# Performance work log

Hardware: AMD Instinct MI355X
Metric: run time of the kernel (lower is better)

The kernel has to match this reference:

```python
import jax, jax.numpy as jnp
import numpy as np

M_MOL = 8192      # number of molecules
A_ATOMS = 32      # atoms per molecule (uniform ragged groups)
N_FEAT = 128      # schnet n_atom_basis


def setup_inputs() -> dict:
    key = jax.random.key(0)
    sr = jax.random.normal(key, (M_MOL * A_ATOMS, N_FEAT), dtype=jnp.float32)
    # idx_m: sorted molecule index per atom, uniform group sizes
    idx_m = jnp.repeat(jnp.arange(M_MOL, dtype=jnp.int32), A_ATOMS)
    return {"scalar_representation": sr, "idx_m": idx_m}


def reference(scalar_representation, idx_m):
    # maxm = int(idx_m[-1]) + 1 in the torch code; groups are uniform here so
    # torch.split over bincount == a simple reshape into [M, A, F].
    maxm = int(idx_m[-1]) + 1
    n_atoms = scalar_representation.shape[0]
    a = n_atoms // maxm
    sr = scalar_representation.reshape(maxm, a, -1)          # [M, A, F]
    # per-molecule correlation (Gram) matrix: c = sr @ sr.T
    c = jnp.einsum('maf,mbf->mab', sr, sr)                    # [M, A, A]
    # eigvalsh returns ascending eigenvalues; torch code takes [0] (smallest)
    eigvals = jnp.linalg.eigvalsh(c)                          # [M, A]
    return eigvals[:, 0]                                      # [M]
```

## Files before the change

kernel.cpp:

```cpp
#include <hip/hip_runtime.h>
#include <hip/hip_bf16.h>

#define DEVINL __device__ __forceinline__

typedef __attribute__((ext_vector_type(8))) short short8;
typedef __attribute__((ext_vector_type(4))) float f32x4;

DEVINL float rcp_f(float x) { return __builtin_amdgcn_rcpf(x); }

#define LDS_FENCE() __asm__ volatile("" ::: "memory")

template<int CTRL>
DEVINL float dpp_mov(float x) {
  return __int_as_float(__builtin_amdgcn_update_dpp(
      0, __float_as_int(x), CTRL, 0xF, 0xF, true));
}
DEVINL float group_sum(float x) {
  x += dpp_mov<0xB1>(x);
  x += dpp_mov<0x4E>(x);
  x += dpp_mov<0x141>(x);
  x += dpp_mov<0x140>(x);
  return x;
}
DEVINL float group_min(float x) {
  x = fminf(x, dpp_mov<0xB1>(x));
  x = fminf(x, dpp_mov<0x4E>(x));
  x = fminf(x, dpp_mov<0x141>(x));
  x = fminf(x, dpp_mov<0x140>(x));
  return x;
}
DEVINL float group_max(float x) {
  x = fmaxf(x, dpp_mov<0xB1>(x));
  x = fmaxf(x, dpp_mov<0x4E>(x));
  x = fmaxf(x, dpp_mov<0x141>(x));
  x = fmaxf(x, dpp_mov<0x140>(x));
  return x;
}

DEVINL short bf_hi(float f, float& rem) {
  unsigned u = __float_as_uint(f);
  unsigned rh = (u + 0x8000u) >> 16;
  rem = f - __uint_as_float(rh << 16);
  return (short)rh;
}
DEVINL short bf_of(float f) {
  return (short)((__float_as_uint(f) + 0x8000u) >> 16);
}
DEVINL void cvt_hilo(float4 fa, float4 fb, short8& h, short8& lo) {
  float rm;
  h[0] = bf_hi(fa.x, rm); lo[0] = bf_of(rm);
  h[1] = bf_hi(fa.y, rm); lo[1] = bf_of(rm);
  h[2] = bf_hi(fa.z, rm); lo[2] = bf_of(rm);
  h[3] = bf_hi(fa.w, rm); lo[3] = bf_of(rm);
  h[4] = bf_hi(fb.x, rm); lo[4] = bf_of(rm);
  h[5] = bf_hi(fb.y, rm); lo[5] = bf_of(rm);
  h[6] = bf_hi(fb.z, rm); lo[6] = bf_of(rm);
  h[7] = bf_hi(fb.w, rm); lo[7] = bf_of(rm);
}
DEVINL f32x4 mfma_bf16(short8 a, short8 b, f32x4 c) {
  return __builtin_amdgcn_mfma_f32_16x16x32_bf16(a, b, c, 0, 0, 0);
}

template<int K>
DEVINL void house_step(float (&r0)[32], float (&r1)[32], int l, int lane,
                       float* vbuf, float* pbuf, float* dbuf, float* ebuf) {
  constexpr int C0 = (K + 1) / 4;
  constexpr int PE = (K + 1) & 3;

  float xm0, xm1;
  if constexpr (K < 15) xm0 = (l > K) ? r0[K] : 0.0f;
  else                  xm0 = 0.0f;
  if constexpr (K < 16) xm1 = r1[K];
  else                  xm1 = (l > K - 16) ? r1[K] : 0.0f;

  vbuf[l] = xm0; vbuf[l + 16] = xm1;
  LDS_FENCE();

  float xsrc = (K + 1 < 16) ? xm0 : xm1;
  float x0 = __shfl(xsrc, (lane & 48) + ((K + 1) & 15), 64);
  float nn = group_sum(xm0 * xm0 + xm1 * xm1);

  float4 vc[8];
  #pragma unroll
  for (int c = C0; c < 8; ++c) vc[c] = *(const float4*)(vbuf + 4 * c);

  float alpha = -copysignf(sqrtf(nn), x0);
  float denom = nn - alpha * x0;
  float beta = (denom > 1e-20f) ? rcp_f(denom) : 0.0f;

  float v0, v1;
  if constexpr (K + 1 < 16) {
    v0 = xm0 - ((l == K + 1) ? alpha : 0.0f);
    v1 = xm1;
  } else {
    v0 = 0.0f;
    v1 = xm1 - ((l == K + 1 - 16) ? alpha : 0.0f);
  }
  if constexpr (PE == 0)      vc[C0].x -= alpha;
  else if constexpr (PE == 1) vc[C0].y -= alpha;
  else if constexpr (PE == 2) vc[C0].z -= alpha;
  else                        vc[C0].w -= alpha;

  float p0 = 0.0f;
  if constexpr (K < 15) {
    float a0 = 0.0f, a1 = 0.0f;
    #pragma unroll
    for (int c = C0; c < 8; ++c) {
      a0 = fmaf(r0[4 * c + 0], vc[c].x, a0); a1 = fmaf(r0[4 * c + 1], vc[c].y, a1);
      a0 = fmaf(r0[4 * c + 2], vc[c].z, a0); a1 = fmaf(r0[4 * c + 3], vc[c].w, a1);
    }
    p0 = a0 + a1;
  }
  float b0 = 0.0f, b1 = 0.0f;
  #pragma unroll
  for (int c = C0; c < 8; ++c) {
    b0 = fmaf(r1[4 * c + 0], vc[c].x, b0); b1 = fmaf(r1[4 * c + 1], vc[c].y, b1);
    b0 = fmaf(r1[4 * c + 2], vc[c].z, b0); b1 = fmaf(r1[4 * c + 3], vc[c].w, b1);
  }
  float p1 = b0 + b1;

  pbuf[l] = p0; pbuf[l + 16] = p1;
  LDS_FENCE();
  float G = group_sum(v0 * p0 + v1 * p1);
  float c2 = 0.5f * beta * beta * G;

  float s_p0 = 0.0f, s_v0 = 0.0f;
  if constexpr (K < 15) {
    bool act0 = (l > K);
    s_p0 = beta * v0;
    s_v0 = act0 ? fmaf(-2.0f * c2, v0, beta * p0) : 0.0f;
  }
  float s_p1 = beta * v1;
  float s_v1;
  if constexpr (K < 16) s_v1 = fmaf(-2.0f * c2, v1, beta * p1);
  else                  s_v1 = (l > K - 16) ? fmaf(-2.0f * c2, v1, beta * p1) : 0.0f;

  #pragma unroll
  for (int c = C0; c < 8; ++c) {
    float4 pc = *(const float4*)(pbuf + 4 * c);
    if constexpr (K < 15) {
      r0[4 * c + 0] -= s_p0 * pc.x + s_v0 * vc[c].x;
      r0[4 * c + 1] -= s_p0 * pc.y + s_v0 * vc[c].y;
      r0[4 * c + 2] -= s_p0 * pc.z + s_v0 * vc[c].z;
      r0[4 * c + 3] -= s_p0 * pc.w + s_v0 * vc[c].w;
    }
    r1[4 * c + 0] -= s_p1 * pc.x + s_v1 * vc[c].x;
    r1[4 * c + 1] -= s_p1 * pc.y + s_v1 * vc[c].y;
    r1[4 * c + 2] -= s_p1 * pc.z + s_v1 * vc[c].z;
    r1[4 * c + 3] -= s_p1 * pc.w + s_v1 * vc[c].w;
  }

  if constexpr (K < 16) {
    if (l == K) { dbuf[K] = r0[K]; ebuf[K] = alpha; }
  } else {
    if (l == K - 16) { dbuf[K] = r1[K]; ebuf[K] = alpha; }
  }
}

template<int K>
DEVINL void house_all(float (&r0)[32], float (&r1)[32], int l, int lane,
                      float* vbuf, float* pbuf, float* dbuf, float* ebuf) {
  house_step<K>(r0, r1, l, lane, vbuf, pbuf, dbuf, ebuf);
  if constexpr (K < 30) house_all<K + 1>(r0, r1, l, lane, vbuf, pbuf, dbuf, ebuf);
}

__global__ __launch_bounds__(256) void Correlation_85134841741354_kernel(
    const float* __restrict__ A, float* __restrict__ out, int M) {
  const int lane = threadIdx.x & 63;
  const int wave = threadIdx.x >> 6;
  const int q    = lane >> 4;
  const int t    = lane & 15;
  const int molbase = blockIdx.x * 16 + wave * 4;
  if (molbase >= M) return;

  __shared__ float ldsT[4][4][32 * 36 + 8];

  #pragma unroll 1
  for (int g = 0; g < 4; ++g) {
    const float* Am = A + (size_t)(molbase + g) * (32 * 128);
    f32x4 acc00 = {0.f, 0.f, 0.f, 0.f}, acc01 = {0.f, 0.f, 0.f, 0.f};
    f32x4 acc10 = {0.f, 0.f, 0.f, 0.f}, acc11 = {0.f, 0.f, 0.f, 0.f};
    #pragma unroll
    for (int c = 0; c < 4; ++c) {
      const float* pr0 = Am + t * 128        + 32 * c + 8 * q;
      const float* pr1 = Am + (t + 16) * 128 + 32 * c + 8 * q;
      float4 fa0 = *(const float4*)(pr0);
      float4 fb0 = *(const float4*)(pr0 + 4);
      float4 fa1 = *(const float4*)(pr1);
      float4 fb1 = *(const float4*)(pr1 + 4);
      short8 h0, l0, h1, l1;
      cvt_hilo(fa0, fb0, h0, l0);
      cvt_hilo(fa1, fb1, h1, l1);
      acc00 = mfma_bf16(h0, h0, acc00); acc00 = mfma_bf16(h0, l0, acc00); acc00 = mfma_bf16(l0, h0, acc00);
      acc01 = mfma_bf16(h0, h1, acc01); acc01 = mfma_bf16(h0, l1, acc01); acc01 = mfma_bf16(l0, h1, acc01);
      acc10 = mfma_bf16(h1, h0, acc10); acc10 = mfma_bf16(h1, l0, acc10); acc10 = mfma_bf16(l1, h0, acc10);
      acc11 = mfma_bf16(h1, h1, acc11); acc11 = mfma_bf16(h1, l1, acc11); acc11 = mfma_bf16(l1, h1, acc11);
    }
    float* tg = &ldsT[wave][g][0];
    #pragma unroll
    for (int reg = 0; reg < 4; ++reg) {
      tg[(4 * q + reg) * 36 + t]           = acc00[reg];
      tg[(4 * q + reg) * 36 + 16 + t]      = acc01[reg];
      tg[(16 + 4 * q + reg) * 36 + t]      = acc10[reg];
      tg[(16 + 4 * q + reg) * 36 + 16 + t] = acc11[reg];
    }
  }
  LDS_FENCE();

  float* tq = &ldsT[wave][q][0];
  float r0[32], r1[32];
  #pragma unroll
  for (int c = 0; c < 8; ++c) {
    float4 a = *(const float4*)(tq + t * 36 + 4 * c);
    r0[4 * c + 0] = a.x; r0[4 * c + 1] = a.y;
    r0[4 * c + 2] = a.z; r0[4 * c + 3] = a.w;
    float4 b = *(const float4*)(tq + (t + 16) * 36 + 4 * c);
    r1[4 * c + 0] = b.x; r1[4 * c + 1] = b.y;
    r1[4 * c + 2] = b.z; r1[4 * c + 3] = b.w;
  }
  LDS_FENCE();

  float* vbuf = tq;
  float* pbuf = tq + 40;
  float* dbuf = tq + 80;
  float* ebuf = tq + 120;

  house_all<0>(r0, r1, t, lane, vbuf, pbuf, dbuf, ebuf);
  if (t == 15) { dbuf[31] = r1[31]; ebuf[31] = 0.0f; }
  LDS_FENCE();

  float d0 = dbuf[t], d1 = dbuf[t + 16];
  float eh0 = ebuf[t];
  float el0 = (t > 0) ? ebuf[t - 1] : 0.0f;
  float eh1 = ebuf[t + 16];
  float el1 = ebuf[t + 15];
  float rad0 = fabsf(eh0) + fabsf(el0);
  float rad1 = fabsf(eh1) + fabsf(el1);
  float glo = group_min(fminf(d0 - rad0, d1 - rad1));
  float ghi = group_max(fmaxf(d0 + rad0, d1 + rad1));
  float lo = fmaxf(glo - 1e-3f, 0.0f);
  float hi = ghi + 1e-3f;

  float vd[32], ve2[32];
  #pragma unroll
  for (int c = 0; c < 8; ++c) {
    float4 dc = *(const float4*)(dbuf + 4 * c);
    float4 ec = *(const float4*)(ebuf + 4 * c);
    vd[4 * c + 0] = dc.x; vd[4 * c + 1] = dc.y;
    vd[4 * c + 2] = dc.z; vd[4 * c + 3] = dc.w;
    ve2[4 * c + 0] = ec.x * ec.x; ve2[4 * c + 1] = ec.y * ec.y;
    ve2[4 * c + 2] = ec.z * ec.z; ve2[4 * c + 3] = ec.w * ec.w;
  }

  #pragma unroll
  for (int rr = 0; rr < 3; ++rr) {
    float stp = (hi - lo) * (1.0f / 17.0f);
    float sig = fmaf(stp, (float)(t + 1), lo);
    float qq = vd[0] - sig;
    int cnt = (qq < 0.0f) ? 1 : 0;
    #pragma unroll
    for (int i = 1; i < 32; ++i) {
      float qs = (fabsf(qq) < 1e-12f) ? ((qq < 0.0f) ? -1e-12f : 1e-12f) : qq;
      qq = (vd[i] - sig) - ve2[i - 1] * rcp_f(qs);
      cnt += (qq < 0.0f) ? 1 : 0;
    }
    unsigned long long m64 = __ballot(cnt >= 1);
    unsigned hm = (unsigned)((m64 >> (q * 16)) & 0xFFFFu);
    int b = (hm == 0u) ? 16 : (__ffs(hm) - 1);
    float nhi = (b == 16) ? hi : fmaf(stp, (float)(b + 1), lo);
    lo = fmaf(stp, (float)b, lo);
    hi = nhi;
  }

  if (t == 0) out[molbase + q] = 0.5f * (lo + hi);
}

extern "C" void kernel_launch(void* const* d_in, const int* in_sizes, int n_in,
                              void* d_out, int out_size, void* d_ws, size_t ws_size,
                              hipStream_t stream) {
  const float* A = (const float*)d_in[0];
  float* out = (float*)d_out;
  int n_atoms = in_sizes[1];
  int M = n_atoms / 32;
  int blocks = (M + 15) / 16;
  hipLaunchKernelGGL(Correlation_85134841741354_kernel,
                     dim3(blocks), dim3(256), 0, stream, A, out, M);
}
```

Before: 207.3 us.

## Assign one 32-lane half-wave per molecule for tridiagonalization and bisection

Each molecule's 32x32 Gram matrix now goes to 32 lanes, each holding one row, instead of 16 lanes holding two rows. A wave therefore handles 2 molecules instead of 4, and twice as many blocks are launched. Reductions gain a swizzle xor-16 step, and the bisection uses 32 sample points per round instead of 16, which narrows the interval further each round. The goal is to halve the per-lane register and ALU work in the serial Householder chain and to allow higher occupancy via launch_bounds(256,4). The cost is more waves in total and extra cross-lane traffic.

```diff
diff --git a/kernel.cpp b/kernel.cpp
--- a/kernel.cpp
+++ b/kernel.cpp
@@ -14,12 +14,16 @@
 DEVINL float dpp_mov(float x) {
   return __int_as_float(__builtin_amdgcn_update_dpp(
       0, __float_as_int(x), CTRL, 0xF, 0xF, true));
+}
+DEVINL float swz_xor16(float x) {
+  return __int_as_float(__builtin_amdgcn_ds_swizzle(__float_as_int(x), 0x401F));
 }
 DEVINL float group_sum(float x) {
   x += dpp_mov<0xB1>(x);
   x += dpp_mov<0x4E>(x);
   x += dpp_mov<0x141>(x);
   x += dpp_mov<0x140>(x);
+  x += swz_xor16(x);
   return x;
 }
 DEVINL float group_min(float x) {
@@ -27,6 +31,7 @@
   x = fminf(x, dpp_mov<0x4E>(x));
   x = fminf(x, dpp_mov<0x141>(x));
   x = fminf(x, dpp_mov<0x140>(x));
+  x = fminf(x, swz_xor16(x));
   return x;
 }
 DEVINL float group_max(float x) {
@@ -34,6 +39,7 @@
   x = fmaxf(x, dpp_mov<0x4E>(x));
   x = fmaxf(x, dpp_mov<0x141>(x));
   x = fmaxf(x, dpp_mov<0x140>(x));
+  x = fmaxf(x, swz_xor16(x));
   return x;
 }
 
@@ -62,23 +68,17 @@
 }
 
 template<int K>
-DEVINL void house_step(float (&r0)[32], float (&r1)[32], int l, int lane,
+DEVINL void house_step(float (&r)[32], int l, int lane,
                        float* vbuf, float* pbuf, float* dbuf, float* ebuf) {
   constexpr int C0 = (K + 1) / 4;
   constexpr int PE = (K + 1) & 3;
 
-  float xm0, xm1;
-  if constexpr (K < 15) xm0 = (l > K) ? r0[K] : 0.0f;
-  else                  xm0 = 0.0f;
-  if constexpr (K < 16) xm1 = r1[K];
-  else                  xm1 = (l > K - 16) ? r1[K] : 0.0f;
-
-  vbuf[l] = xm0; vbuf[l + 16] = xm1;
-  LDS_FENCE();
-
-  float xsrc = (K + 1 < 16) ? xm0 : xm1;
-  float x0 = __shfl(xsrc, (lane & 48) + ((K + 1) & 15), 64);
-  float nn = group_sum(xm0 * xm0 + xm1 * xm1);
+  float xm = (l > K) ? r[K] : 0.0f;
+  vbuf[l] = xm;
+  LDS_FENCE();
+
+  float x0 = __shfl(xm, (lane & 32) + (K + 1), 64);
+  float nn = group_sum(xm * xm);
 
   float4 vc[8];
   #pragma unroll
@@ -88,95 +88,62 @@
   float denom = nn - alpha * x0;
   float beta = (denom > 1e-20f) ? rcp_f(denom) : 0.0f;
 
-  float v0, v1;
-  if constexpr (K + 1 < 16) {
-    v0 = xm0 - ((l == K + 1) ? alpha : 0.0f);
-    v1 = xm1;
-  } else {
-    v0 = 0.0f;
-    v1 = xm1 - ((l == K + 1 - 16) ? alpha : 0.0f);
-  }
+  float v = xm - ((l == K + 1) ? alpha : 0.0f);
   if constexpr (PE == 0)      vc[C0].x -= alpha;
   else if constexpr (PE == 1) vc[C0].y -= alpha;
   else if constexpr (PE == 2) vc[C0].z -= alpha;
   else                        vc[C0].w -= alpha;
 
-  float p0 = 0.0f;
-  if constexpr (K < 15) {
-    float a0 = 0.0f, a1 = 0.0f;
-    #pragma unroll
-    for (int c = C0; c < 8; ++c) {
-      a0 = fmaf(r0[4 * c + 0], vc[c].x, a0); a1 = fmaf(r0[4 * c + 1], vc[c].y, a1);
-      a0 = fmaf(r0[4 * c + 2], vc[c].z, a0); a1 = fmaf(r0[4 * c + 3], vc[c].w, a1);
-    }
-    p0 = a0 + a1;
-  }
-  float b0 = 0.0f, b1 = 0.0f;
+  float a0 = 0.0f, a1 = 0.0f;
   #pragma unroll
   for (int c = C0; c < 8; ++c) {
-    b0 = fmaf(r1[4 * c + 0], vc[c].x, b0); b1 = fmaf(r1[4 * c + 1], vc[c].y, b1);
-    b0 = fmaf(r1[4 * c + 2], vc[c].z, b0); b1 = fmaf(r1[4 * c + 3], vc[c].w, b1);
-  }
-  float p1 = b0 + b1;
-
-  pbuf[l] = p0; pbuf[l + 16] = p1;
-  LDS_FENCE();
-  float G = group_sum(v0 * p0 + v1 * p1);
+    a0 = fmaf(r[4 * c + 0], vc[c].x, a0); a1 = fmaf(r[4 * c + 1], vc[c].y, a1);
+    a0 = fmaf(r[4 * c + 2], vc[c].z, a0); a1 = fmaf(r[4 * c + 3], vc[c].w, a1);
+  }
+  float p = a0 + a1;
+
+  pbuf[l] = p;
+  LDS_FENCE();
+  float G = group_sum(v * p);
   float c2 = 0.5f * beta * beta * G;
 
-  float s_p0 = 0.0f, s_v0 = 0.0f;
-  if constexpr (K < 15) {
-    bool act0 = (l > K);
-    s_p0 = beta * v0;
-    s_v0 = act0 ? fmaf(-2.0f * c2, v0, beta * p0) : 0.0f;
-  }
-  float s_p1 = beta * v1;
-  float s_v1;
-  if constexpr (K < 16) s_v1 = fmaf(-2.0f * c2, v1, beta * p1);
-  else                  s_v1 = (l > K - 16) ? fmaf(-2.0f * c2, v1, beta * p1) : 0.0f;
+  float s_p = beta * v;
+  float s_v = (l > K) ? fmaf(-2.0f * c2, v, beta * p) : 0.0f;
 
   #pragma unroll
   for (int c = C0; c < 8; ++c) {
     float4 pc = *(const float4*)(pbuf + 4 * c);
-    if constexpr (K < 15) {
-      r0[4 * c + 0] -= s_p0 * pc.x + s_v0 * vc[c].x;
-      r0[4 * c + 1] -= s_p0 * pc.y + s_v0 * vc[c].y;
-      r0[4 * c + 2] -= s_p0 * pc.z + s_v0 * vc[c].z;
-      r0[4 * c + 3] -= s_p0 * pc.w + s_v0 * vc[c].w;
-    }
-    r1[4 * c + 0] -= s_p1 * pc.x + s_v1 * vc[c].x;
-    r1[4 * c + 1] -= s_p1 * pc.y + s_v1 * vc[c].y;
-    r1[4 * c + 2] -= s_p1 * pc.z + s_v1 * vc[c].z;
-    r1[4 * c + 3] -= s_p1 * pc.w + s_v1 * vc[c].w;
-  }
-
-  if constexpr (K < 16) {
-    if (l == K) { dbuf[K] = r0[K]; ebuf[K] = alpha; }
-  } else {
-    if (l == K - 16) { dbuf[K] = r1[K]; ebuf[K] = alpha; }
-  }
+    r[4 * c + 0] -= s_p * pc.x + s_v * vc[c].x;
+    r[4 * c + 1] -= s_p * pc.y + s_v * vc[c].y;
+    r[4 * c + 2] -= s_p * pc.z + s_v * vc[c].z;
+    r[4 * c + 3] -= s_p * pc.w + s_v * vc[c].w;
+  }
+
+  if (l == K) { dbuf[K] = r[K]; ebuf[K] = alpha; }
 }
 
 template<int K>
-DEVINL void house_all(float (&r0)[32], float (&r1)[32], int l, int lane,
+DEVINL void house_all(float (&r)[32], int l, int lane,
                       float* vbuf, float* pbuf, float* dbuf, float* ebuf) {
-  house_step<K>(r0, r1, l, lane, vbuf, pbuf, dbuf, ebuf);
-  if constexpr (K < 30) house_all<K + 1>(r0, r1, l, lane, vbuf, pbuf, dbuf, ebuf);
-}
-
-__global__ __launch_bounds__(256) void Correlation_85134841741354_kernel(
+  house_step<K>(r, l, lane, vbuf, pbuf, dbuf, ebuf);
+  if constexpr (K < 30) house_all<K + 1>(r, l, lane, vbuf, pbuf, dbuf, ebuf);
+}
+
+__global__ __launch_bounds__(256, 4) void Correlation_85134841741354_kernel(
     const float* __restrict__ A, float* __restrict__ out, int M) {
   const int lane = threadIdx.x & 63;
   const int wave = threadIdx.x >> 6;
   const int q    = lane >> 4;
   const int t    = lane & 15;
-  const int molbase = blockIdx.x * 16 + wave * 4;
+  const int a    = lane >> 5;
+  const int l    = lane & 31;
+  const int molbase = blockIdx.x * 8 + wave * 2;
   if (molbase >= M) return;
 
-  __shared__ float ldsT[4][4][32 * 36 + 8];
+  __shared__ float ldsT[4][2][32 * 36 + 8];
 
   #pragma unroll 1
-  for (int g = 0; g < 4; ++g) {
+  for (int g = 0; g < 2; ++g) {
     const float* Am = A + (size_t)(molbase + g) * (32 * 128);
     f32x4 acc00 = {0.f, 0.f, 0.f, 0.f}, acc01 = {0.f, 0.f, 0.f, 0.f};
     f32x4 acc10 = {0.f, 0.f, 0.f, 0.f}, acc11 = {0.f, 0.f, 0.f, 0.f};
@@ -207,16 +174,13 @@
   }
   LDS_FENCE();
 
-  float* tq = &ldsT[wave][q][0];
-  float r0[32], r1[32];
+  float* tq = &ldsT[wave][a][0];
+  float r[32];
   #pragma unroll
   for (int c = 0; c < 8; ++c) {
-    float4 a = *(const float4*)(tq + t * 36 + 4 * c);
-    r0[4 * c + 0] = a.x; r0[4 * c + 1] = a.y;
-    r0[4 * c + 2] = a.z; r0[4 * c + 3] = a.w;
-    float4 b = *(const float4*)(tq + (t + 16) * 36 + 4 * c);
-    r1[4 * c + 0] = b.x; r1[4 * c + 1] = b.y;
-    r1[4 * c + 2] = b.z; r1[4 * c + 3] = b.w;
+    float4 x = *(const float4*)(tq + l * 36 + 4 * c);
+    r[4 * c + 0] = x.x; r[4 * c + 1] = x.y;
+    r[4 * c + 2] = x.z; r[4 * c + 3] = x.w;
   }
   LDS_FENCE();
 
@@ -225,19 +189,16 @@
   float* dbuf = tq + 80;
   float* ebuf = tq + 120;
 
-  house_all<0>(r0, r1, t, lane, vbuf, pbuf, dbuf, ebuf);
-  if (t == 15) { dbuf[31] = r1[31]; ebuf[31] = 0.0f; }
-  LDS_FENCE();
-
-  float d0 = dbuf[t], d1 = dbuf[t + 16];
-  float eh0 = ebuf[t];
-  float el0 = (t > 0) ? ebuf[t - 1] : 0.0f;
-  float eh1 = ebuf[t + 16];
-  float el1 = ebuf[t + 15];
-  float rad0 = fabsf(eh0) + fabsf(el0);
-  float rad1 = fabsf(eh1) + fabsf(el1);
-  float glo = group_min(fminf(d0 - rad0, d1 - rad1));
-  float ghi = group_max(fmaxf(d0 + rad0, d1 + rad1));
+  house_all<0>(r, l, lane, vbuf, pbuf, dbuf, ebuf);
+  if (l == 31) { dbuf[31] = r[31]; ebuf[31] = 0.0f; }
+  LDS_FENCE();
+
+  float d  = dbuf[l];
+  float eh = ebuf[l];
+  float el = (l > 0) ? ebuf[l - 1] : 0.0f;
+  float rad = fabsf(eh) + fabsf(el);
+  float glo = group_min(d - rad);
+  float ghi = group_max(d + rad);
   float lo = fmaxf(glo - 1e-3f, 0.0f);
   float hi = ghi + 1e-3f;
 
@@ -254,8 +215,8 @@
 
   #pragma unroll
   for (int rr = 0; rr < 3; ++rr) {
-    float stp = (hi - lo) * (1.0f / 17.0f);
-    float sig = fmaf(stp, (float)(t + 1), lo);
+    float stp = (hi - lo) * (1.0f / 33.0f);
+    float sig = fmaf(stp, (float)(l + 1), lo);
     float qq = vd[0] - sig;
     int cnt = (qq < 0.0f) ? 1 : 0;
     #pragma unroll
@@ -265,14 +226,14 @@
       cnt += (qq < 0.0f) ? 1 : 0;
     }
     unsigned long long m64 = __ballot(cnt >= 1);
-    unsigned hm = (unsigned)((m64 >> (q * 16)) & 0xFFFFu);
-    int b = (hm == 0u) ? 16 : (__ffs(hm) - 1);
-    float nhi = (b == 16) ? hi : fmaf(stp, (float)(b + 1), lo);
+    unsigned hm = (unsigned)(m64 >> (a * 32));
+    int b = (hm == 0u) ? 32 : (__ffs(hm) - 1);
+    float nhi = (b == 32) ? hi : fmaf(stp, (float)(b + 1), lo);
     lo = fmaf(stp, (float)b, lo);
     hi = nhi;
   }
 
-  if (t == 0) out[molbase + q] = 0.5f * (lo + hi);
+  if (l == 0) out[molbase + a] = 0.5f * (lo + hi);
 }
 
 extern "C" void kernel_launch(void* const* d_in, const int* in_sizes, int n_in,
@@ -282,7 +243,7 @@
   float* out = (float*)d_out;
   int n_atoms = in_sizes[1];
   int M = n_atoms / 32;
-  int blocks = (M + 15) / 16;
+  int blocks = (M + 7) / 8;
   hipLaunchKernelGGL(Correlation_85134841741354_kernel,
                      dim3(blocks), dim3(256), 0, stream, A, out, M);
 }
```

Measured after the change: 215.6 us. 1.04x slower.
